# Kernel optimization log

Measured on AMD Instinct MI355X. Metric: run time of the kernel, lower is better.

Reference implementation:

```python
import jax, jax.numpy as jnp
import numpy as np

TOKENS, H, I = 2048, 3584, 18944


def setup_inputs() -> dict:
    key = jax.random.key(0)
    ks = jax.random.split(key, 8)
    x = jax.random.normal(ks[0], (TOKENS, H), dtype=jnp.float32)
    gate_w = jax.random.randint(ks[1], (I, H), -127, 128, dtype=jnp.int32).astype(jnp.int8)
    up_w = jax.random.randint(ks[2], (I, H), -127, 128, dtype=jnp.int32).astype(jnp.int8)
    down_w = jax.random.randint(ks[3], (H, I), -127, 128, dtype=jnp.int32).astype(jnp.int8)
    # realistic small per-tensor scales
    gate_w_scale = jnp.float32(0.01) * (jnp.float32(0.5) + jax.random.uniform(ks[4], ()))
    up_w_scale = jnp.float32(0.01) * (jnp.float32(0.5) + jax.random.uniform(ks[5], ()))
    down_w_scale = jnp.float32(0.01) * (jnp.float32(0.5) + jax.random.uniform(ks[6], ()))
    down_input_scale = jnp.float32(0.05) * (jnp.float32(0.5) + jax.random.uniform(ks[7], ()))
    return {"x": x, "gate_w": gate_w, "up_w": up_w, "down_w": down_w,
            "gate_w_scale": gate_w_scale, "up_w_scale": up_w_scale,
            "down_w_scale": down_w_scale, "down_input_scale": down_input_scale}


def _quant_per_token(x):
    # dynamic per-token symmetric int8 quantization
    s = jnp.max(jnp.abs(x), axis=-1, keepdims=True) / jnp.float32(127.0)
    s = jnp.maximum(s, jnp.float32(1e-8))
    q = jnp.clip(jnp.round(x / s), -127, 127).astype(jnp.int8)
    return q, s  # q: [T, K] int8, s: [T, 1] fp32


def _int8_gemm(q, w):
    # q: [T, K] int8, w: [N, K] int8 -> [T, N] int32 accumulate
    return jax.lax.dot(q, w.T, preferred_element_type=jnp.int32)


def reference(x, gate_w, up_w, down_w, gate_w_scale, up_w_scale,
              down_w_scale, down_input_scale):
    # fc1 (gate & up): per-token dynamic activation quant, shared quantized input
    qx, sx = _quant_per_token(x)
    gate = _int8_gemm(qx, gate_w).astype(jnp.float32) * sx * gate_w_scale  # [T, I]
    up = _int8_gemm(qx, up_w).astype(jnp.float32) * sx * up_w_scale        # [T, I]
    h = jax.nn.silu(gate) * up  # SwiGLU, fp32
    # fc2 (down): static per-tensor activation quant with stored input scale
    qh = jnp.clip(jnp.round(h / down_input_scale), -127, 127).astype(jnp.int8)
    out = _int8_gemm(qh, down_w).astype(jnp.float32) * (down_input_scale * down_w_scale)
    return out  # [T, H] fp32
```

## Files before the change

kernel.cpp:

```cpp
#include <hip/hip_runtime.h>
#include <stdint.h>

#define TOKENS 2048
#define H_DIM 3584
#define I_DIM 18944

typedef int v4i __attribute__((ext_vector_type(4)));

__device__ __forceinline__ void async_copy16(const void* g, void* lds) {
    __builtin_amdgcn_global_load_lds(
        (const __attribute__((address_space(1))) void*)g,
        (__attribute__((address_space(3))) void*)lds,
        16, 0, 0);
}


__global__ __launch_bounds__(256)
void pack_kernel(const int* __restrict__ src, int8_t* __restrict__ dst, int n4) {
    int i = blockIdx.x * 256 + threadIdx.x;
    if (i >= n4) return;
    v4i w = ((const v4i*)src)[i];
    int packed = (w.x & 0xff) | ((w.y & 0xff) << 8) |
                 ((w.z & 0xff) << 16) | (w.w << 24);
    ((int*)dst)[i] = packed;
}

__global__ __launch_bounds__(256)
void quant_x_kernel(const float* __restrict__ x,
                    int8_t* __restrict__ qx,
                    float* __restrict__ sx) {
    const int row = blockIdx.x;
    const float* xr = x + (size_t)row * H_DIM;
    float m = 0.0f;
    for (int j = threadIdx.x; j < H_DIM; j += 256)
        m = fmaxf(m, fabsf(xr[j]));
    for (int off = 32; off > 0; off >>= 1)
        m = fmaxf(m, __shfl_down(m, off, 64));
    __shared__ float wmax[4];
    if ((threadIdx.x & 63) == 0) wmax[threadIdx.x >> 6] = m;
    __syncthreads();
    float mm = fmaxf(fmaxf(wmax[0], wmax[1]), fmaxf(wmax[2], wmax[3]));
    float s = fmaxf(mm / 127.0f, 1e-8f);
    if (threadIdx.x == 0) sx[row] = s;
    for (int j = threadIdx.x; j < H_DIM; j += 256) {
        float q = rintf(xr[j] / s);
        q = fminf(fmaxf(q, -127.0f), 127.0f);
        qx[(size_t)row * H_DIM + j] = (int8_t)q;
    }
}

__global__ __launch_bounds__(256)
void fc1_kernel(const int8_t* __restrict__ qx,
                const float* __restrict__ sx,
                const int8_t* __restrict__ gw,
                const int8_t* __restrict__ uw,
                const float* __restrict__ gws,
                const float* __restrict__ uws,
                const float* __restrict__ dis,
                int8_t* __restrict__ qh) {
    __shared__ __align__(16) int8_t ldsA[128 * 128];
    __shared__ __align__(16) int8_t ldsG[64 * 128];
    __shared__ __align__(16) int8_t ldsU[64 * 128];

    const int tid  = threadIdx.x;
    const int wave = tid >> 6;
    const int lane = tid & 63;
    const int n0 = blockIdx.x * 64;
    const int m0 = blockIdx.y * 128;

    const int rowS  = tid >> 3;
    const int kOffS = (((tid & 7) ^ ((tid >> 3) & 7))) * 16;
    const int8_t* gA = qx + (size_t)(m0 + rowS) * H_DIM + kOffS;
    const int8_t* gG = gw + (size_t)(n0 + rowS) * H_DIM + kOffS;
    const int8_t* gU = uw + (size_t)(n0 + rowS) * H_DIM + kOffS;
    int8_t* lA = ldsA + tid * 16;
    int8_t* lG = ldsG + tid * 16;
    int8_t* lU = ldsU + tid * 16;

    const int fr = lane & 15;
    const int fq = lane >> 4;

    v4i accG[2][4] = {};
    v4i accU[2][4] = {};

    for (int k0 = 0; k0 < H_DIM; k0 += 128) {
        __syncthreads();
#pragma unroll
        for (int j = 0; j < 4; ++j)
            async_copy16(gA + k0 + (size_t)(32 * j) * H_DIM, lA + j * 4096);
#pragma unroll
        for (int j = 0; j < 2; ++j) {
            async_copy16(gG + k0 + (size_t)(32 * j) * H_DIM, lG + j * 4096);
            async_copy16(gU + k0 + (size_t)(32 * j) * H_DIM, lU + j * 4096);
        }
        __syncthreads();
#pragma unroll
        for (int kh = 0; kh < 2; ++kh) {
            const int sw = ((kh * 4 + fq) ^ (fr & 7)) * 16;
            v4i a0 = *(const v4i*)(ldsA + (wave * 32 + fr) * 128 + sw);
            v4i a1 = *(const v4i*)(ldsA + (wave * 32 + 16 + fr) * 128 + sw);
#pragma unroll
            for (int n = 0; n < 4; ++n) {
                v4i bg = *(const v4i*)(ldsG + (n * 16 + fr) * 128 + sw);
                v4i bu = *(const v4i*)(ldsU + (n * 16 + fr) * 128 + sw);
                accG[0][n] = __builtin_amdgcn_mfma_i32_16x16x64_i8(a0, bg, accG[0][n], 0, 0, 0);
                accG[1][n] = __builtin_amdgcn_mfma_i32_16x16x64_i8(a1, bg, accG[1][n], 0, 0, 0);
                accU[0][n] = __builtin_amdgcn_mfma_i32_16x16x64_i8(a0, bu, accU[0][n], 0, 0, 0);
                accU[1][n] = __builtin_amdgcn_mfma_i32_16x16x64_i8(a1, bu, accU[1][n], 0, 0, 0);
            }
        }
    }

    const float gscale = *gws;
    const float uscale = *uws;
    const float dis_v  = *dis;

#pragma unroll
    for (int m = 0; m < 2; ++m) {
#pragma unroll
        for (int r = 0; r < 4; ++r) {
            const int row = m0 + wave * 32 + m * 16 + fq * 4 + r;
            const float s  = sx[row];
            const float gs = s * gscale;
            const float us = s * uscale;
            const size_t base = (size_t)row * I_DIM + n0;
#pragma unroll
            for (int n = 0; n < 4; ++n) {
                float g = (float)accG[m][n][r] * gs;
                float u = (float)accU[m][n][r] * us;
                float h = (g / (1.0f + expf(-g))) * u;
                float q = rintf(h / dis_v);
                q = fminf(fmaxf(q, -127.0f), 127.0f);
                qh[base + n * 16 + fr] = (int8_t)q;
            }
        }
    }
}

__global__ __launch_bounds__(256)
void fc2_kernel(const int8_t* __restrict__ qh,
                const int8_t* __restrict__ dw,
                const float* __restrict__ dws,
                const float* __restrict__ dis,
                float* __restrict__ out) {
    __shared__ __align__(16) int8_t ldsA[128 * 128];
    __shared__ __align__(16) int8_t ldsW[64 * 128];

    const int tid  = threadIdx.x;
    const int wave = tid >> 6;
    const int lane = tid & 63;
    const int n0 = blockIdx.x * 64;
    const int m0 = blockIdx.y * 128;

    const int rowS  = tid >> 3;
    const int kOffS = (((tid & 7) ^ ((tid >> 3) & 7))) * 16;
    const int8_t* gA = qh + (size_t)(m0 + rowS) * I_DIM + kOffS;
    const int8_t* gW = dw + (size_t)(n0 + rowS) * I_DIM + kOffS;
    int8_t* lA = ldsA + tid * 16;
    int8_t* lW = ldsW + tid * 16;

    const int fr = lane & 15;
    const int fq = lane >> 4;

    v4i acc[2][4] = {};

    for (int k0 = 0; k0 < I_DIM; k0 += 128) {
        __syncthreads();
#pragma unroll
        for (int j = 0; j < 4; ++j)
            async_copy16(gA + k0 + (size_t)(32 * j) * I_DIM, lA + j * 4096);
#pragma unroll
        for (int j = 0; j < 2; ++j)
            async_copy16(gW + k0 + (size_t)(32 * j) * I_DIM, lW + j * 4096);
        __syncthreads();
#pragma unroll
        for (int kh = 0; kh < 2; ++kh) {
            const int sw = ((kh * 4 + fq) ^ (fr & 7)) * 16;
            v4i a0 = *(const v4i*)(ldsA + (wave * 32 + fr) * 128 + sw);
            v4i a1 = *(const v4i*)(ldsA + (wave * 32 + 16 + fr) * 128 + sw);
#pragma unroll
            for (int n = 0; n < 4; ++n) {
                v4i b = *(const v4i*)(ldsW + (n * 16 + fr) * 128 + sw);
                acc[0][n] = __builtin_amdgcn_mfma_i32_16x16x64_i8(a0, b, acc[0][n], 0, 0, 0);
                acc[1][n] = __builtin_amdgcn_mfma_i32_16x16x64_i8(a1, b, acc[1][n], 0, 0, 0);
            }
        }
    }

    const float sc = (*dis) * (*dws);
#pragma unroll
    for (int m = 0; m < 2; ++m)
#pragma unroll
        for (int n = 0; n < 4; ++n)
#pragma unroll
            for (int r = 0; r < 4; ++r) {
                const int row = m0 + wave * 32 + m * 16 + fq * 4 + r;
                const int col = n0 + n * 16 + fr;
                out[(size_t)row * H_DIM + col] = (float)acc[m][n][r] * sc;
            }
}

extern "C" void kernel_launch(void* const* d_in, const int* in_sizes, int n_in,
                              void* d_out, int out_size, void* d_ws, size_t ws_size,
                              hipStream_t stream) {
    const float* x    = (const float*)d_in[0];
    const int*   gw32 = (const int*)d_in[1];
    const int*   uw32 = (const int*)d_in[2];
    const int*   dw32 = (const int*)d_in[3];
    const float* gws  = (const float*)d_in[4];
    const float* uws  = (const float*)d_in[5];
    const float* dws  = (const float*)d_in[6];
    const float* dis  = (const float*)d_in[7];
    float* out = (float*)d_out;

    const size_t W = (size_t)I_DIM * H_DIM;
    int8_t* qx  = (int8_t*)d_ws;
    float*  sx  = (float*)((char*)d_ws + (size_t)TOKENS * H_DIM);
    int8_t* qh  = (int8_t*)((char*)d_ws + (size_t)TOKENS * H_DIM + TOKENS * 4);
    int8_t* gw8 = (int8_t*)((char*)d_ws + (size_t)TOKENS * H_DIM + TOKENS * 4
                            + (size_t)TOKENS * I_DIM);
    int8_t* uw8 = gw8 + W;
    int8_t* dw8 = uw8 + W;

    const int n4 = (int)(W / 4);
    const int packBlocks = (n4 + 255) / 256;
    pack_kernel<<<packBlocks, 256, 0, stream>>>(gw32, gw8, n4);
    pack_kernel<<<packBlocks, 256, 0, stream>>>(uw32, uw8, n4);
    pack_kernel<<<packBlocks, 256, 0, stream>>>(dw32, dw8, n4);

    quant_x_kernel<<<TOKENS, 256, 0, stream>>>(x, qx, sx);

    dim3 g1(I_DIM / 64, TOKENS / 128);
    fc1_kernel<<<g1, 256, 0, stream>>>(qx, sx, gw8, uw8, gws, uws, dis, qh);

    dim3 g2(H_DIM / 64, TOKENS / 128);
    fc2_kernel<<<g2, 256, 0, stream>>>(qh, dw8, dws, dis, out);
}
```

Measured before the change: 1.277 ms.

## Enlarge GEMM tiles with double-buffered LDS pipelining and vectorize pre-kernels

Both GEMM kernels are rebuilt. fc1 now uses 256x128 tiles with 512 threads and fc2 uses 128x128 tiles. Each has double-buffered LDS with async prefetch of the next K tile, MFMA phases split by barriers under raised priority, and an XCD-aware block-index remap. The three weight-pack launches are merged into one kernel, and the activation quantization is vectorized with float4 loads and packed int8 stores. The goals are more data reuse per tile, overlap of global loads with compute, and fewer launches. In exchange, register and LDS pressure rise and occupancy may drop.

```diff
diff --git a/kernel.cpp b/kernel.cpp
--- a/kernel.cpp
+++ b/kernel.cpp
@@ -16,9 +16,16 @@
 
 
 __global__ __launch_bounds__(256)
-void pack_kernel(const int* __restrict__ src, int8_t* __restrict__ dst, int n4) {
-    int i = blockIdx.x * 256 + threadIdx.x;
-    if (i >= n4) return;
+void pack3_kernel(const int* __restrict__ s0, int8_t* __restrict__ d0,
+                  const int* __restrict__ s1, int8_t* __restrict__ d1,
+                  const int* __restrict__ s2, int8_t* __restrict__ d2,
+                  int pb) {
+    int b = blockIdx.x;
+    const int* src; int8_t* dst;
+    if (b >= 2 * pb)    { src = s2; dst = d2; b -= 2 * pb; }
+    else if (b >= pb)   { src = s1; dst = d1; b -= pb; }
+    else                { src = s0; dst = d0; }
+    const int i = b * 256 + threadIdx.x;
     v4i w = ((const v4i*)src)[i];
     int packed = (w.x & 0xff) | ((w.y & 0xff) << 8) |
                  ((w.z & 0xff) << 16) | (w.w << 24);
@@ -30,10 +37,13 @@
                     int8_t* __restrict__ qx,
                     float* __restrict__ sx) {
     const int row = blockIdx.x;
-    const float* xr = x + (size_t)row * H_DIM;
+    const float4* xr = (const float4*)(x + (size_t)row * H_DIM);
     float m = 0.0f;
-    for (int j = threadIdx.x; j < H_DIM; j += 256)
-        m = fmaxf(m, fabsf(xr[j]));
+    for (int j = threadIdx.x; j < 896; j += 256) {
+        float4 v = xr[j];
+        m = fmaxf(m, fmaxf(fmaxf(fabsf(v.x), fabsf(v.y)),
+                           fmaxf(fabsf(v.z), fabsf(v.w))));
+    }
     for (int off = 32; off > 0; off >>= 1)
         m = fmaxf(m, __shfl_down(m, off, 64));
     __shared__ float wmax[4];
@@ -42,14 +52,44 @@
     float mm = fmaxf(fmaxf(wmax[0], wmax[1]), fmaxf(wmax[2], wmax[3]));
     float s = fmaxf(mm / 127.0f, 1e-8f);
     if (threadIdx.x == 0) sx[row] = s;
-    for (int j = threadIdx.x; j < H_DIM; j += 256) {
-        float q = rintf(xr[j] / s);
-        q = fminf(fmaxf(q, -127.0f), 127.0f);
-        qx[(size_t)row * H_DIM + j] = (int8_t)q;
-    }
-}
-
-__global__ __launch_bounds__(256)
+    int* qrow = (int*)(qx + (size_t)row * H_DIM);
+    for (int j = threadIdx.x; j < 896; j += 256) {
+        float4 v = xr[j];
+        int q0 = (int)fminf(fmaxf(rintf(v.x / s), -127.0f), 127.0f);
+        int q1 = (int)fminf(fmaxf(rintf(v.y / s), -127.0f), 127.0f);
+        int q2 = (int)fminf(fmaxf(rintf(v.z / s), -127.0f), 127.0f);
+        int q3 = (int)fminf(fmaxf(rintf(v.w / s), -127.0f), 127.0f);
+        qrow[j] = (q0 & 0xff) | ((q1 & 0xff) << 8) | ((q2 & 0xff) << 16) |
+                  (q3 << 24);
+    }
+}
+
+#define FC1_LOADA(MH) do { _Pragma("unroll")                                   \
+  for (int m_ = 0; m_ < 4; ++m_) {                                             \
+    a[m_][0] = *(const v4i*)(Ab + aOff + (MH)*8192 + m_*2048 + sw0);           \
+    a[m_][1] = *(const v4i*)(Ab + aOff + (MH)*8192 + m_*2048 + sw1);           \
+  } } while (0)
+
+#define FC1_LOADB(NF) do {                                                     \
+    bg[NF][0] = *(const v4i*)(Bb + bOff + (NF)*2048 + sw0);                    \
+    bg[NF][1] = *(const v4i*)(Bb + bOff + (NF)*2048 + sw1);                    \
+    bu[NF][0] = *(const v4i*)(Bb + 16384 + bOff + (NF)*2048 + sw0);            \
+    bu[NF][1] = *(const v4i*)(Bb + 16384 + bOff + (NF)*2048 + sw1);            \
+  } while (0)
+
+#define FC1_MFMA(MH, NF) do { _Pragma("unroll")                                \
+  for (int m_ = 0; m_ < 4; ++m_) {                                             \
+    accG[(MH)*4+m_][NF] = __builtin_amdgcn_mfma_i32_16x16x64_i8(               \
+        a[m_][0], bg[NF][0], accG[(MH)*4+m_][NF], 0, 0, 0);                    \
+    accU[(MH)*4+m_][NF] = __builtin_amdgcn_mfma_i32_16x16x64_i8(               \
+        a[m_][0], bu[NF][0], accU[(MH)*4+m_][NF], 0, 0, 0);                    \
+    accG[(MH)*4+m_][NF] = __builtin_amdgcn_mfma_i32_16x16x64_i8(               \
+        a[m_][1], bg[NF][1], accG[(MH)*4+m_][NF], 0, 0, 0);                    \
+    accU[(MH)*4+m_][NF] = __builtin_amdgcn_mfma_i32_16x16x64_i8(               \
+        a[m_][1], bu[NF][1], accU[(MH)*4+m_][NF], 0, 0, 0);                    \
+  } } while (0)
+
+__global__ __launch_bounds__(512, 2)
 void fc1_kernel(const int8_t* __restrict__ qx,
                 const float* __restrict__ sx,
                 const int8_t* __restrict__ gw,
@@ -58,57 +98,96 @@
                 const float* __restrict__ uws,
                 const float* __restrict__ dis,
                 int8_t* __restrict__ qh) {
-    __shared__ __align__(16) int8_t ldsA[128 * 128];
-    __shared__ __align__(16) int8_t ldsG[64 * 128];
-    __shared__ __align__(16) int8_t ldsU[64 * 128];
+    __shared__ __align__(16) int8_t lds[2][65536];
 
     const int tid  = threadIdx.x;
     const int wave = tid >> 6;
     const int lane = tid & 63;
-    const int n0 = blockIdx.x * 64;
-    const int m0 = blockIdx.y * 128;
+    const int wr = wave >> 2;
+    const int wc = wave & 3;
+    const int fr = lane & 15;
+    const int fq = lane >> 4;
+
+    const int bid = blockIdx.x;
+    const int gid = (bid & 7) * 148 + (bid >> 3);
+    const int m0 = (gid & 7) * 256;
+    const int n0 = (gid >> 3) * 128;
 
     const int rowS  = tid >> 3;
-    const int kOffS = (((tid & 7) ^ ((tid >> 3) & 7))) * 16;
+    const int kOffS = ((tid & 7) ^ (rowS & 7)) * 16;
     const int8_t* gA = qx + (size_t)(m0 + rowS) * H_DIM + kOffS;
     const int8_t* gG = gw + (size_t)(n0 + rowS) * H_DIM + kOffS;
     const int8_t* gU = uw + (size_t)(n0 + rowS) * H_DIM + kOffS;
-    int8_t* lA = ldsA + tid * 16;
-    int8_t* lG = ldsG + tid * 16;
-    int8_t* lU = ldsU + tid * 16;
-
-    const int fr = lane & 15;
-    const int fq = lane >> 4;
-
-    v4i accG[2][4] = {};
-    v4i accU[2][4] = {};
-
-    for (int k0 = 0; k0 < H_DIM; k0 += 128) {
+
+    const int sw0 = (fq ^ (fr & 7)) * 16;
+    const int sw1 = ((4 + fq) ^ (fr & 7)) * 16;
+    const int aOff = (wr * 128 + fr) * 128;
+    const int bOff = (wc * 32 + fr) * 128;
+
+    v4i accG[8][2] = {};
+    v4i accU[8][2] = {};
+    v4i a[4][2], bg[2][2], bu[2][2];
+
+    {
+        int8_t* lA = &lds[0][tid * 16];
+        int8_t* lB = &lds[0][32768 + tid * 16];
+#pragma unroll
+        for (int j = 0; j < 4; ++j)
+            async_copy16(gA + (size_t)(64 * j) * H_DIM, lA + j * 8192);
+        async_copy16(gG,                         lB);
+        async_copy16(gG + (size_t)64 * H_DIM,    lB + 8192);
+        async_copy16(gU,                         lB + 16384);
+        async_copy16(gU + (size_t)64 * H_DIM,    lB + 24576);
+    }
+    __syncthreads();
+
+    for (int kt = 0; kt < H_DIM / 128; ++kt) {
+        const int8_t* Ab = lds[kt & 1];
+        const int8_t* Bb = Ab + 32768;
+        int8_t* An = (int8_t*)lds[(kt & 1) ^ 1];
+        int8_t* Bn = An + 32768;
+        const bool pf = (kt + 1) < (H_DIM / 128);
+        const int  kN = (kt + 1) * 128;
+
+        if (pf) {
+            int8_t* lA = An + tid * 16;
+#pragma unroll
+            for (int j = 0; j < 4; ++j)
+                async_copy16(gA + kN + (size_t)(64 * j) * H_DIM, lA + j * 8192);
+        }
+        FC1_LOADA(0);
+        FC1_LOADB(0);
+        __builtin_amdgcn_s_barrier();
+        __builtin_amdgcn_s_setprio(1);
+        FC1_MFMA(0, 0);
+        __builtin_amdgcn_s_setprio(0);
+        __builtin_amdgcn_s_barrier();
+
+        if (pf) {
+            int8_t* lB = Bn + tid * 16;
+            async_copy16(gG + kN,                      lB);
+            async_copy16(gG + kN + (size_t)64 * H_DIM, lB + 8192);
+            async_copy16(gU + kN,                      lB + 16384);
+            async_copy16(gU + kN + (size_t)64 * H_DIM, lB + 24576);
+        }
+        FC1_LOADB(1);
+        __builtin_amdgcn_s_barrier();
+        __builtin_amdgcn_s_setprio(1);
+        FC1_MFMA(0, 1);
+        __builtin_amdgcn_s_setprio(0);
+        __builtin_amdgcn_s_barrier();
+
+        FC1_LOADA(1);
+        __builtin_amdgcn_s_barrier();
+        __builtin_amdgcn_s_setprio(1);
+        FC1_MFMA(1, 0);
+        __builtin_amdgcn_s_setprio(0);
+        __builtin_amdgcn_s_barrier();
+
+        __builtin_amdgcn_s_setprio(1);
+        FC1_MFMA(1, 1);
+        __builtin_amdgcn_s_setprio(0);
         __syncthreads();
-#pragma unroll
-        for (int j = 0; j < 4; ++j)
-            async_copy16(gA + k0 + (size_t)(32 * j) * H_DIM, lA + j * 4096);
-#pragma unroll
-        for (int j = 0; j < 2; ++j) {
-            async_copy16(gG + k0 + (size_t)(32 * j) * H_DIM, lG + j * 4096);
-            async_copy16(gU + k0 + (size_t)(32 * j) * H_DIM, lU + j * 4096);
-        }
-        __syncthreads();
-#pragma unroll
-        for (int kh = 0; kh < 2; ++kh) {
-            const int sw = ((kh * 4 + fq) ^ (fr & 7)) * 16;
-            v4i a0 = *(const v4i*)(ldsA + (wave * 32 + fr) * 128 + sw);
-            v4i a1 = *(const v4i*)(ldsA + (wave * 32 + 16 + fr) * 128 + sw);
-#pragma unroll
-            for (int n = 0; n < 4; ++n) {
-                v4i bg = *(const v4i*)(ldsG + (n * 16 + fr) * 128 + sw);
-                v4i bu = *(const v4i*)(ldsU + (n * 16 + fr) * 128 + sw);
-                accG[0][n] = __builtin_amdgcn_mfma_i32_16x16x64_i8(a0, bg, accG[0][n], 0, 0, 0);
-                accG[1][n] = __builtin_amdgcn_mfma_i32_16x16x64_i8(a1, bg, accG[1][n], 0, 0, 0);
-                accU[0][n] = __builtin_amdgcn_mfma_i32_16x16x64_i8(a0, bu, accU[0][n], 0, 0, 0);
-                accU[1][n] = __builtin_amdgcn_mfma_i32_16x16x64_i8(a1, bu, accU[1][n], 0, 0, 0);
-            }
-        }
     }
 
     const float gscale = *gws;
@@ -116,87 +195,136 @@
     const float dis_v  = *dis;
 
 #pragma unroll
-    for (int m = 0; m < 2; ++m) {
+    for (int M = 0; M < 8; ++M) {
 #pragma unroll
         for (int r = 0; r < 4; ++r) {
-            const int row = m0 + wave * 32 + m * 16 + fq * 4 + r;
+            const int row = m0 + wr * 128 + M * 16 + fq * 4 + r;
             const float s  = sx[row];
             const float gs = s * gscale;
             const float us = s * uscale;
-            const size_t base = (size_t)row * I_DIM + n0;
-#pragma unroll
-            for (int n = 0; n < 4; ++n) {
-                float g = (float)accG[m][n][r] * gs;
-                float u = (float)accU[m][n][r] * us;
+            const size_t base = (size_t)row * I_DIM + n0 + wc * 32;
+#pragma unroll
+            for (int nf = 0; nf < 2; ++nf) {
+                float g = (float)accG[M][nf][r] * gs;
+                float u = (float)accU[M][nf][r] * us;
                 float h = (g / (1.0f + expf(-g))) * u;
                 float q = rintf(h / dis_v);
                 q = fminf(fmaxf(q, -127.0f), 127.0f);
-                qh[base + n * 16 + fr] = (int8_t)q;
+                qh[base + nf * 16 + fr] = (int8_t)q;
             }
         }
     }
 }
 
-__global__ __launch_bounds__(256)
+#define FC2_LOADA() do { _Pragma("unroll")                                     \
+  for (int m_ = 0; m_ < 4; ++m_) {                                             \
+    a[m_][0] = *(const v4i*)(Ab + aOff + m_*2048 + sw0);                       \
+    a[m_][1] = *(const v4i*)(Ab + aOff + m_*2048 + sw1);                       \
+  } } while (0)
+
+#define FC2_LOADB(NH) do { _Pragma("unroll")                                   \
+  for (int n_ = 0; n_ < 2; ++n_) {                                             \
+    b[n_][0] = *(const v4i*)(Bb + bOff + ((NH)*2+n_)*2048 + sw0);              \
+    b[n_][1] = *(const v4i*)(Bb + bOff + ((NH)*2+n_)*2048 + sw1);              \
+  } } while (0)
+
+#define FC2_MFMA(NH) do { _Pragma("unroll")                                    \
+  for (int m_ = 0; m_ < 4; ++m_) { _Pragma("unroll")                           \
+    for (int n_ = 0; n_ < 2; ++n_) {                                           \
+      acc[m_][(NH)*2+n_] = __builtin_amdgcn_mfma_i32_16x16x64_i8(              \
+          a[m_][0], b[n_][0], acc[m_][(NH)*2+n_], 0, 0, 0);                    \
+      acc[m_][(NH)*2+n_] = __builtin_amdgcn_mfma_i32_16x16x64_i8(              \
+          a[m_][1], b[n_][1], acc[m_][(NH)*2+n_], 0, 0, 0);                    \
+    } } } while (0)
+
+__global__ __launch_bounds__(256, 2)
 void fc2_kernel(const int8_t* __restrict__ qh,
                 const int8_t* __restrict__ dw,
                 const float* __restrict__ dws,
                 const float* __restrict__ dis,
                 float* __restrict__ out) {
-    __shared__ __align__(16) int8_t ldsA[128 * 128];
-    __shared__ __align__(16) int8_t ldsW[64 * 128];
+    __shared__ __align__(16) int8_t lds[2][32768];
 
     const int tid  = threadIdx.x;
     const int wave = tid >> 6;
     const int lane = tid & 63;
-    const int n0 = blockIdx.x * 64;
-    const int m0 = blockIdx.y * 128;
+    const int wr = wave >> 1;
+    const int wc = wave & 1;
+    const int fr = lane & 15;
+    const int fq = lane >> 4;
+
+    const int bid = blockIdx.x;
+    const int gid = (bid & 7) * 56 + (bid >> 3);
+    const int m0 = (gid & 15) * 128;
+    const int n0 = (gid >> 4) * 128;
 
     const int rowS  = tid >> 3;
-    const int kOffS = (((tid & 7) ^ ((tid >> 3) & 7))) * 16;
+    const int kOffS = ((tid & 7) ^ (rowS & 7)) * 16;
     const int8_t* gA = qh + (size_t)(m0 + rowS) * I_DIM + kOffS;
     const int8_t* gW = dw + (size_t)(n0 + rowS) * I_DIM + kOffS;
-    int8_t* lA = ldsA + tid * 16;
-    int8_t* lW = ldsW + tid * 16;
-
-    const int fr = lane & 15;
-    const int fq = lane >> 4;
-
-    v4i acc[2][4] = {};
-
-    for (int k0 = 0; k0 < I_DIM; k0 += 128) {
+
+    const int sw0 = (fq ^ (fr & 7)) * 16;
+    const int sw1 = ((4 + fq) ^ (fr & 7)) * 16;
+    const int aOff = (wr * 64 + fr) * 128;
+    const int bOff = (wc * 64 + fr) * 128;
+
+    v4i acc[4][4] = {};
+    v4i a[4][2], b[2][2];
+
+    {
+        int8_t* lA = &lds[0][tid * 16];
+        int8_t* lB = &lds[0][16384 + tid * 16];
+#pragma unroll
+        for (int j = 0; j < 4; ++j) {
+            async_copy16(gA + (size_t)(32 * j) * I_DIM, lA + j * 4096);
+            async_copy16(gW + (size_t)(32 * j) * I_DIM, lB + j * 4096);
+        }
+    }
+    __syncthreads();
+
+    for (int kt = 0; kt < I_DIM / 128; ++kt) {
+        const int8_t* Ab = lds[kt & 1];
+        const int8_t* Bb = Ab + 16384;
+        int8_t* An = (int8_t*)lds[(kt & 1) ^ 1];
+        int8_t* Bn = An + 16384;
+        const bool pf = (kt + 1) < (I_DIM / 128);
+        const int  kN = (kt + 1) * 128;
+
+        if (pf) {
+            int8_t* lA = An + tid * 16;
+            int8_t* lB = Bn + tid * 16;
+#pragma unroll
+            for (int j = 0; j < 4; ++j) {
+                async_copy16(gA + kN + (size_t)(32 * j) * I_DIM, lA + j * 4096);
+                async_copy16(gW + kN + (size_t)(32 * j) * I_DIM, lB + j * 4096);
+            }
+        }
+        FC2_LOADA();
+        FC2_LOADB(0);
+        __builtin_amdgcn_s_barrier();
+        __builtin_amdgcn_s_setprio(1);
+        FC2_MFMA(0);
+        __builtin_amdgcn_s_setprio(0);
+        __builtin_amdgcn_s_barrier();
+
+        FC2_LOADB(1);
+        __builtin_amdgcn_s_barrier();
+        __builtin_amdgcn_s_setprio(1);
+        FC2_MFMA(1);
+        __builtin_amdgcn_s_setprio(0);
         __syncthreads();
-#pragma unroll
-        for (int j = 0; j < 4; ++j)
-            async_copy16(gA + k0 + (size_t)(32 * j) * I_DIM, lA + j * 4096);
-#pragma unroll
-        for (int j = 0; j < 2; ++j)
-            async_copy16(gW + k0 + (size_t)(32 * j) * I_DIM, lW + j * 4096);
-        __syncthreads();
-#pragma unroll
-        for (int kh = 0; kh < 2; ++kh) {
-            const int sw = ((kh * 4 + fq) ^ (fr & 7)) * 16;
-            v4i a0 = *(const v4i*)(ldsA + (wave * 32 + fr) * 128 + sw);
-            v4i a1 = *(const v4i*)(ldsA + (wave * 32 + 16 + fr) * 128 + sw);
-#pragma unroll
-            for (int n = 0; n < 4; ++n) {
-                v4i b = *(const v4i*)(ldsW + (n * 16 + fr) * 128 + sw);
-                acc[0][n] = __builtin_amdgcn_mfma_i32_16x16x64_i8(a0, b, acc[0][n], 0, 0, 0);
-                acc[1][n] = __builtin_amdgcn_mfma_i32_16x16x64_i8(a1, b, acc[1][n], 0, 0, 0);
-            }
-        }
     }
 
     const float sc = (*dis) * (*dws);
 #pragma unroll
-    for (int m = 0; m < 2; ++m)
-#pragma unroll
-        for (int n = 0; n < 4; ++n)
+    for (int m_ = 0; m_ < 4; ++m_)
+#pragma unroll
+        for (int n_ = 0; n_ < 4; ++n_)
 #pragma unroll
             for (int r = 0; r < 4; ++r) {
-                const int row = m0 + wave * 32 + m * 16 + fq * 4 + r;
-                const int col = n0 + n * 16 + fr;
-                out[(size_t)row * H_DIM + col] = (float)acc[m][n][r] * sc;
+                const int row = m0 + wr * 64 + m_ * 16 + fq * 4 + r;
+                const int col = n0 + wc * 64 + n_ * 16 + fr;
+                out[(size_t)row * H_DIM + col] = (float)acc[m_][n_][r] * sc;
             }
 }
 
@@ -222,17 +350,14 @@
     int8_t* uw8 = gw8 + W;
     int8_t* dw8 = uw8 + W;
 
-    const int n4 = (int)(W / 4);
-    const int packBlocks = (n4 + 255) / 256;
-    pack_kernel<<<packBlocks, 256, 0, stream>>>(gw32, gw8, n4);
-    pack_kernel<<<packBlocks, 256, 0, stream>>>(uw32, uw8, n4);
-    pack_kernel<<<packBlocks, 256, 0, stream>>>(dw32, dw8, n4);
+    const int pb = (int)(W / 4 / 256);
+    pack3_kernel<<<3 * pb, 256, 0, stream>>>(gw32, gw8, uw32, uw8, dw32, dw8, pb);
 
     quant_x_kernel<<<TOKENS, 256, 0, stream>>>(x, qx, sx);
 
-    dim3 g1(I_DIM / 64, TOKENS / 128);
-    fc1_kernel<<<g1, 256, 0, stream>>>(qx, sx, gw8, uw8, gws, uws, dis, qh);
-
-    dim3 g2(H_DIM / 64, TOKENS / 128);
-    fc2_kernel<<<g2, 256, 0, stream>>>(qh, dw8, dws, dis, out);
-}
+    fc1_kernel<<<(TOKENS / 256) * (I_DIM / 128), 512, 0, stream>>>(
+        qx, sx, gw8, uw8, gws, uws, dis, qh);
+
+    fc2_kernel<<<(TOKENS / 128) * (H_DIM / 128), 256, 0, stream>>>(
+        qh, dw8, dws, dis, out);
+}
```

New measurement: 1.157 ms. -9.5%, faster.
